# Kernel tuning notes

Measured on AMD Instinct MI355X. Metric: run time of the kernel, lower is better.

Reference implementation:

```python
import jax, jax.numpy as jnp
import numpy as np

B, S, E, H = 2, 2048, 768, 12
HD = E // H  # 64


def setup_inputs() -> dict:
    rng = jax.random.key(0)
    ks = jax.random.split(rng, 11)
    std = 0.02
    return {
        "query": jax.random.normal(ks[0], (B, S, E), dtype=jnp.float32),
        "key": jax.random.normal(ks[1], (B, S, E), dtype=jnp.float32),
        "value": jax.random.normal(ks[2], (B, S, E), dtype=jnp.float32),
        # weights stored as (in, out) so projection is x @ W + b
        "Wq": jax.random.normal(ks[3], (E, E), dtype=jnp.float32) * std,
        "bq": jax.random.normal(ks[4], (E,), dtype=jnp.float32) * std,
        "Wk": jax.random.normal(ks[5], (E, E), dtype=jnp.float32) * std,
        "bk": jax.random.normal(ks[6], (E,), dtype=jnp.float32) * std,
        "Wv": jax.random.normal(ks[7], (E, E), dtype=jnp.float32) * std,
        "bv": jax.random.normal(ks[8], (E,), dtype=jnp.float32) * std,
        "Wo": jax.random.normal(ks[9], (E, E), dtype=jnp.float32) * std,
        "bo": jax.random.normal(ks[10], (E,), dtype=jnp.float32) * std,
    }


def reference(query, key, value, Wq, bq, Wk, bk, Wv, bv, Wo, bo):
    bsz, tgt_len, embed_dim = query.shape
    src_len = key.shape[1]
    q = query @ Wq + bq  # [B, T, E]
    k = key @ Wk + bk    # [B, S, E]
    v = value @ Wv + bv  # [B, S, E]
    # Faithful replication of torch .view(bsz*H, len, head_dim) on a
    # (bsz, len, E)-contiguous tensor: plain row-major reshape (NOT a
    # transpose-based head split).
    q = q.reshape(bsz * H, tgt_len, HD)
    k = k.reshape(bsz * H, src_len, HD)
    v = v.reshape(bsz * H, src_len, HD)
    scale = 1.0 / (HD ** 0.5)
    scores = jnp.einsum('bqd,bkd->bqk', q, k) * scale  # [B*H, T, S]
    attn = jax.nn.softmax(scores, axis=-1)
    # is_causal=True: mask applied AFTER softmax (rows no longer normalized)
    attn = jnp.tril(attn)
    out = jnp.einsum('bqk,bkd->bqd', attn, v)  # [B*H, T, HD]
    out = out.reshape(bsz, tgt_len, embed_dim)
    return out @ Wo + bo
```

## Files before the change

kernel.cpp:

```cpp
#include <hip/hip_runtime.h>
#include <hip/hip_bf16.h>


typedef __bf16 bf16;
typedef __attribute__((ext_vector_type(4))) __bf16 bf16x4;
typedef __attribute__((ext_vector_type(8))) __bf16 bf16x8;
typedef __attribute__((ext_vector_type(4))) float f32x4;
typedef __attribute__((ext_vector_type(16))) float f32x16;
typedef __attribute__((ext_vector_type(4))) unsigned int uint4v;

#define MFMA16(a,b,c) __builtin_amdgcn_mfma_f32_16x16x32_bf16((a),(b),(c),0,0,0)
#define MFMA32(a,b,c) __builtin_amdgcn_mfma_f32_32x32x16_bf16((a),(b),(c),0,0,0)

typedef const __attribute__((address_space(1))) unsigned int GU32;
typedef __attribute__((address_space(3))) unsigned int LU32;

__device__ __forceinline__ void gll16(const void* gsrc, void* ldst) {
    __builtin_amdgcn_global_load_lds((GU32*)gsrc, (LU32*)ldst, 16, 0, 0);
}

__device__ __forceinline__ unsigned pk_bf16(float lo, float hi) {
    unsigned r;
    asm("v_cvt_pk_bf16_f32 %0, %1, %2" : "=v"(r) : "v"(lo), "v"(hi));
    return r;
}

__device__ __forceinline__ void plane32swap(unsigned &a, unsigned &b) {
    asm("v_permlane32_swap_b32 %0, %1" : "+v"(a), "+v"(b));
}

__device__ __forceinline__ bf16x8 frag_words(unsigned w0, unsigned w1, unsigned w2, unsigned w3) {
    union { unsigned u[4]; bf16x8 v; } f;
    f.u[0] = w0; f.u[1] = w1; f.u[2] = w2; f.u[3] = w3;
    return f.v;
}

__global__ __launch_bounds__(256) void cvt_qkv(
    const float* __restrict__ q, const float* __restrict__ k, const float* __restrict__ v,
    bf16* __restrict__ Qb, bf16* __restrict__ Kb, bf16* __restrict__ Vb)
{
    const float* src = blockIdx.y == 0 ? q : blockIdx.y == 1 ? k : v;
    bf16* dst = blockIdx.y == 0 ? Qb : blockIdx.y == 1 ? Kb : Vb;
    const size_t base = (size_t)blockIdx.x * 2048 + (size_t)threadIdx.x * 8;
    f32x4 lo = *(const f32x4*)&src[base];
    f32x4 hi = *(const f32x4*)&src[base + 4];
    bf16x8 o;
    for (int j = 0; j < 4; ++j) { o[j] = (bf16)lo[j]; o[4 + j] = (bf16)hi[j]; }
    *(bf16x8*)&dst[base] = o;
}

struct TArg { const float* in; bf16* out; };

__global__ __launch_bounds__(256) void transpose_w(TArg a0, TArg a1, TArg a2, TArg a3) {
    TArg ta = blockIdx.z == 0 ? a0 : blockIdx.z == 1 ? a1 : blockIdx.z == 2 ? a2 : a3;
    __shared__ bf16 tile[64][72];
    const int bx = blockIdx.x % 12, by = blockIdx.x / 12;
    const int k0 = by * 64, n0 = bx * 64;
    const int tid = threadIdx.x;
    for (int q = 0; q < 2; ++q) {
        int idx = q * 256 + tid;
        int i = idx >> 3, j0 = (idx & 7) * 8;
        const float* src = &ta.in[(size_t)(k0 + i) * 768 + n0 + j0];
        f32x4 lo = *(const f32x4*)&src[0];
        f32x4 hi = *(const f32x4*)&src[4];
        bf16x8 v;
        for (int j = 0; j < 4; ++j) { v[j] = (bf16)lo[j]; v[4 + j] = (bf16)hi[j]; }
        *(bf16x8*)&tile[i][j0] = v;
    }
    __syncthreads();
    for (int q = 0; q < 2; ++q) {
        int idx = q * 256 + tid;
        int n = idx >> 3, j0 = (idx & 7) * 8;
        bf16x8 v;
        for (int jj = 0; jj < 8; ++jj) v[jj] = tile[j0 + jj][n];
        *(bf16x8*)&ta.out[(size_t)(n0 + n) * 768 + k0 + j0] = v;
    }
}

__global__ __launch_bounds__(256) void vtrans(const bf16* __restrict__ Vp, bf16* __restrict__ Vt) {
    __shared__ bf16 tile[64][72];
    const int g = blockIdx.y;
    const int k0 = blockIdx.x * 64;
    const bf16* src = Vp + (size_t)g * 131072;
    bf16* dst = Vt + (size_t)g * 131072;
    const int tid = threadIdx.x;
    for (int q = 0; q < 2; ++q) {
        int idx = q * 256 + tid;
        int r = idx >> 3, c = (idx & 7) * 8;
        *(uint4v*)&tile[r][c] = *(const uint4v*)&src[(size_t)(k0 + r) * 64 + c];
    }
    __syncthreads();
    for (int q = 0; q < 2; ++q) {
        int idx = q * 256 + tid;
        int d = idx >> 3, c = (idx & 7) * 8;
        bf16x8 v;
        for (int j = 0; j < 8; ++j) v[j] = tile[c + j][d];
        *(bf16x8*)&dst[(size_t)d * 2048 + k0 + c] = v;
    }
}

struct GArg { const bf16* A; const bf16* Bt; const float* bias; void* C; float scale; };

template<int MODE>
__global__ __launch_bounds__(256) void gemm_bt_bias(GArg g0, GArg g1, GArg g2) {
    const int flat = blockIdx.x + 6 * blockIdx.y + 192 * blockIdx.z;
    const int xcd = flat & 7;
    const int idx = flat >> 3;
    const int mat = idx / 24;
    const int rem = idx % 24;
    const int rloc = rem / 6, colb = rem % 6;
    GArg ga = mat == 0 ? g0 : mat == 1 ? g1 : g2;
    const int K = 768, N = 768;
    __shared__ bf16 As[2][128][64];
    __shared__ bf16 Bs[2][128][64];
    const int tid = threadIdx.x;
    const int lane = tid & 63, wave = tid >> 6;
    const int l15 = lane & 15, lg = lane >> 4;
    const int r0 = (xcd * 4 + rloc) * 128, c0 = colb * 128;
    const int wr = (wave >> 1) * 64, wc = (wave & 1) * 64;
    f32x4 acc[4][4] = {};

    const int grow = wave * 8 + (lane >> 3);
    const int gcol = 8 * ((lane & 7) ^ (lane >> 3));

    auto stage = [&](int kt, int buf) {
        for (int i = 0; i < 4; ++i)
            gll16(&ga.A[(size_t)(r0 + i * 32 + grow) * K + kt + gcol], &As[buf][i * 32 + wave * 8][0]);
        for (int i = 0; i < 4; ++i)
            gll16(&ga.Bt[(size_t)(c0 + i * 32 + grow) * K + kt + gcol], &Bs[buf][i * 32 + wave * 8][0]);
    };

    stage(0, 0);
    __syncthreads();

    for (int c = 0; c < 12; ++c) {
        const int buf = c & 1;
        if (c < 11) stage((c + 1) * 64, buf ^ 1);
        for (int kk = 0; kk < 2; ++kk) {
            bf16x8 af[4], bfr[4];
            for (int i = 0; i < 4; ++i) {
                int row = wr + i * 16 + l15;
                af[i] = *(const bf16x8*)&As[buf][row][(kk * 32 + lg * 8) ^ ((row & 7) * 8)];
            }
            for (int j = 0; j < 4; ++j) {
                int row = wc + j * 16 + l15;
                bfr[j] = *(const bf16x8*)&Bs[buf][row][(kk * 32 + lg * 8) ^ ((row & 7) * 8)];
            }
            __builtin_amdgcn_s_setprio(1);
            for (int i = 0; i < 4; ++i)
                for (int j = 0; j < 4; ++j)
                    acc[i][j] = MFMA16(af[i], bfr[j], acc[i][j]);
            __builtin_amdgcn_s_setprio(0);
        }
        __syncthreads();
    }
    for (int j = 0; j < 4; ++j) {
        int col = c0 + wc + j * 16 + l15;
        float bv = ga.bias[col];
        for (int i = 0; i < 4; ++i) {
            int row = r0 + wr + i * 16 + lg * 4;
            for (int r = 0; r < 4; ++r) {
                float val = (acc[i][j][r] + bv) * ga.scale;
                if constexpr (MODE == 0)
                    ((bf16*)ga.C)[(size_t)(row + r) * N + col] = (bf16)val;
                else
                    ((float*)ga.C)[(size_t)(row + r) * N + col] = val;
            }
        }
    }
}

__global__ __launch_bounds__(256, 3) void attn_kernel(
    const bf16* __restrict__ Qp, const bf16* __restrict__ Kp,
    const bf16* __restrict__ Vtg, bf16* __restrict__ Ob)
{
    const int bid = blockIdx.x;
    const int xcd = bid & 7;
    const int idx = bid >> 3;
    const int t = idx & 31, s = idx >> 5;
    const int bx = (s == 0) ? (31 - t)
                 : (s == 1) ? ((15 - t) & 31)
                 : (((t << 1) & 31) | (t >> 4));
    const int g = xcd * 3 + s;
    const int t0 = bx * 64;
    const int tid = threadIdx.x, lane = tid & 63, w = tid >> 6;
    const int wq = w >> 1, p = w & 1;
    const int l31 = lane & 31, hi = lane >> 5;

    if (s == 1) __builtin_amdgcn_s_sleep(8);
    else if (s == 2) __builtin_amdgcn_s_sleep(16);

    __shared__ __align__(16) char smem[32768];
    bf16* KsE = (bf16*)smem;
    bf16* VsE = (bf16*)(smem + 16384);

    const bf16* Qg = Qp + (size_t)g * 131072;
    const bf16* Kg = Kp + (size_t)g * 131072;
    const bf16* Vg = Vtg + (size_t)g * 131072;
    bf16* Og = Ob + (size_t)g * 131072;

    const int qrow = t0 + wq * 32 + l31;
    bf16x8 qB[4];
    for (int m = 0; m < 4; ++m)
        qB[m] = *(const bf16x8*)&Qg[(size_t)qrow * 64 + m * 16 + hi * 8];

    const int srow = w * 16 + (lane >> 3);
    const int scol = 8 * ((lane & 7) ^ (lane >> 3));
    auto stageK = [&](int ch, int b2) {
        const bf16* src = &Kg[(size_t)(ch * 64 + srow) * 64 + scol];
        bf16* dst = KsE + b2 * 4096 + w * 16 * 64;
        gll16(src, dst);
        gll16(src + 8 * 64, dst + 8 * 64);
    };
    auto stageV = [&](int ch, int b2) {
        const bf16* src = &Vg[(size_t)srow * 2048 + ch * 64 + scol];
        bf16* dst = VsE + b2 * 4096 + w * 16 * 64;
        gll16(src, dst);
        gll16(src + 8 * 2048, dst + 8 * 64);
    };

    stageK(0, 0);
    stageV(0, 0);

    f32x16 oacc0 = {}, oacc1 = {};
    float dsum = 0.f;
    const int qmax = t0 + wq * 32 + 31;
    const int qmin = t0 + wq * 32;
    const int kofs = p * 32;
    const int swz = (l31 & 7) * 8;

    int koff[4], voff0[2], voff1[2];
    for (int m = 0; m < 4; ++m)
        koff[m] = (kofs + l31) * 64 + ((m * 16 + hi * 8) ^ swz);
    for (int kt = 0; kt < 2; ++kt) {
        const int col = (kofs + kt * 16 + hi * 8) ^ swz;
        voff0[kt] = l31 * 64 + col;
        voff1[kt] = (32 + l31) * 64 + col;
    }

    for (int c = 0; c < 32; ++c) {
        const int boff = (c & 1) * 4096;
        asm volatile("s_waitcnt vmcnt(0)" ::: "memory");
        __builtin_amdgcn_s_barrier();
        __builtin_amdgcn_sched_barrier(0);
        if (c < 31) {
            stageK(c + 1, (c & 1) ^ 1);
            if (c + 1 <= bx) stageV(c + 1, (c & 1) ^ 1);
        }
        __builtin_amdgcn_sched_barrier(0);

        const int kc = c * 64;
        const bool activ = (kc + kofs <= qmax);
        const bool fullc = (kc + kofs + 31 <= qmin);

        f32x16 s2 = {};
        __builtin_amdgcn_s_setprio(1);
        for (int m = 0; m < 4; ++m) {
            bf16x8 kf = *(const bf16x8*)&KsE[boff + koff[m]];
            s2 = MFMA32(kf, qB[m], s2);
        }
        __builtin_amdgcn_s_setprio(0);

        float e[16];
        for (int r = 0; r < 16; ++r) e[r] = __builtin_exp2f(s2[r]);
        {
            float p01 = e[0] + e[1],  p23 = e[2] + e[3];
            float p45 = e[4] + e[5],  p67 = e[6] + e[7];
            float p89 = e[8] + e[9],  pab = e[10] + e[11];
            float pcd = e[12] + e[13], pef = e[14] + e[15];
            float q0 = p01 + p23, q1 = p45 + p67, q2 = p89 + pab, q3 = pcd + pef;
            dsum += (q0 + q1) + (q2 + q3);
        }

        if (activ) {
            if (!fullc) {
                for (int r = 0; r < 16; ++r) {
                    int kg = kc + kofs + (r & 3) + 8 * (r >> 2) + 4 * hi;
                    if (kg > qrow) e[r] = 0.f;
                }
            }
            bf16x8 pf[2];
            {
                unsigned a0 = pk_bf16(e[0], e[1]), a1 = pk_bf16(e[2], e[3]);
                unsigned b0 = pk_bf16(e[4], e[5]), b1 = pk_bf16(e[6], e[7]);
                plane32swap(a0, b0); plane32swap(a1, b1);
                pf[0] = frag_words(a0, a1, b0, b1);
                a0 = pk_bf16(e[8], e[9]);   a1 = pk_bf16(e[10], e[11]);
                b0 = pk_bf16(e[12], e[13]); b1 = pk_bf16(e[14], e[15]);
                plane32swap(a0, b0); plane32swap(a1, b1);
                pf[1] = frag_words(a0, a1, b0, b1);
            }
            __builtin_amdgcn_s_setprio(1);
            for (int kt = 0; kt < 2; ++kt) {
                bf16x8 v0 = *(const bf16x8*)&VsE[boff + voff0[kt]];
                bf16x8 v1 = *(const bf16x8*)&VsE[boff + voff1[kt]];
                oacc0 = MFMA32(pf[kt], v0, oacc0);
                oacc1 = MFMA32(pf[kt], v1, oacc1);
            }
            __builtin_amdgcn_s_setprio(0);
        }
    }

    dsum += __shfl_xor(dsum, 32);

    __syncthreads();
    float* Ored = (float*)smem;
    float* dred = (float*)(smem + 16384);
    if (l31 == lane) dred[w * 32 + l31] = dsum;
    if (p == 1) {
        float* Op = Ored + wq * 2048;
        for (int r = 0; r < 16; ++r) {
            const int qoff = (r & 3) + 8 * (r >> 2) + 4 * hi;
            Op[qoff * 64 + l31]      = oacc0[r];
            Op[qoff * 64 + 32 + l31] = oacc1[r];
        }
    }
    __syncthreads();
    if (p == 0) {
        const float dtot = dsum + dred[(w + 1) * 32 + l31];
        const float rall = 1.0f / dtot;
        const float* Op = Ored + wq * 2048;
        for (int r = 0; r < 16; ++r) {
            const int qoff = (r & 3) + 8 * (r >> 2) + 4 * hi;
            const float inv = __shfl(rall, qoff);
            const size_t row = (size_t)(t0 + wq * 32 + qoff) * 64;
            Og[row + l31]      = (bf16)((oacc0[r] + Op[qoff * 64 + l31])      * inv);
            Og[row + 32 + l31] = (bf16)((oacc1[r] + Op[qoff * 64 + 32 + l31]) * inv);
        }
    }
}

extern "C" void kernel_launch(void* const* d_in, const int* in_sizes, int n_in,
                              void* d_out, int out_size, void* d_ws, size_t ws_size,
                              hipStream_t stream) {
    const float* query = (const float*)d_in[0];
    const float* key_  = (const float*)d_in[1];
    const float* value = (const float*)d_in[2];
    const float* Wq = (const float*)d_in[3];
    const float* bq = (const float*)d_in[4];
    const float* Wk = (const float*)d_in[5];
    const float* bk = (const float*)d_in[6];
    const float* Wv = (const float*)d_in[7];
    const float* bv = (const float*)d_in[8];
    const float* Wo = (const float*)d_in[9];
    const float* bo = (const float*)d_in[10];
    float* out = (float*)d_out;

    const size_t MN = (size_t)4096 * 768;
    const size_t WW = (size_t)768 * 768;
    bf16* Qp  = (bf16*)d_ws;
    bf16* Kp  = Qp + MN;
    bf16* Vp  = Kp + MN;
    bf16* Obf = Vp + MN;
    bf16* Vtg = Obf + MN;
    bf16* WtQ = Vtg + MN;
    bf16* WtK = WtQ + WW;
    bf16* WtV = WtK + WW;
    bf16* WtO = WtV + WW;
    bf16* Vb  = WtO + WW;
    bf16* Qb  = Obf;
    bf16* Kb  = Vtg;

    cvt_qkv<<<dim3(1536, 3), 256, 0, stream>>>(query, key_, value, Qb, Kb, Vb);

    transpose_w<<<dim3(144, 1, 4), 256, 0, stream>>>(
        TArg{Wq, WtQ}, TArg{Wk, WtK}, TArg{Wv, WtV}, TArg{Wo, WtO});

    gemm_bt_bias<0><<<dim3(6, 32, 3), 256, 0, stream>>>(
        GArg{Qb, WtQ, bq, Qp, 0.18033688f},
        GArg{Kb, WtK, bk, Kp, 1.0f},
        GArg{Vb, WtV, bv, Vp, 1.0f});

    vtrans<<<dim3(32, 24), 256, 0, stream>>>(Vp, Vtg);

    attn_kernel<<<dim3(768), 256, 0, stream>>>(Qp, Kp, Vtg, Obf);

    gemm_bt_bias<1><<<dim3(6, 32, 1), 256, 0, stream>>>(
        GArg{Obf, WtO, bo, out, 1.0f},
        GArg{Obf, WtO, bo, out, 1.0f},
        GArg{Obf, WtO, bo, out, 1.0f});
}
```

Baseline: 107.2 us.

## Merge input conversion and weight transpose kernels; fuse V transpose into projection epilogue

The separate fp32-to-bf16 conversion and weight-transpose kernels are merged into a single prelude launch that dispatches on block index. The V-projection GEMM epilogue now writes directly in the transposed per-head layout the attention kernel expects, removing the standalone vtrans kernel. This saves two launches and one full read and write of V. The transposed epilogue stores are scattered 2-byte writes with a stride of 2048 elements, so they are poorly coalesced.

```diff
diff --git a/kernel.cpp b/kernel.cpp
--- a/kernel.cpp
+++ b/kernel.cpp
@@ -35,71 +35,54 @@
     return f.v;
 }
 
-__global__ __launch_bounds__(256) void cvt_qkv(
+struct TArg { const float* in; bf16* out; };
+
+__global__ __launch_bounds__(256) void prelude(
     const float* __restrict__ q, const float* __restrict__ k, const float* __restrict__ v,
-    bf16* __restrict__ Qb, bf16* __restrict__ Kb, bf16* __restrict__ Vb)
+    bf16* __restrict__ Qb, bf16* __restrict__ Kb, bf16* __restrict__ Vb,
+    TArg a0, TArg a1, TArg a2, TArg a3)
 {
-    const float* src = blockIdx.y == 0 ? q : blockIdx.y == 1 ? k : v;
-    bf16* dst = blockIdx.y == 0 ? Qb : blockIdx.y == 1 ? Kb : Vb;
-    const size_t base = (size_t)blockIdx.x * 2048 + (size_t)threadIdx.x * 8;
-    f32x4 lo = *(const f32x4*)&src[base];
-    f32x4 hi = *(const f32x4*)&src[base + 4];
-    bf16x8 o;
-    for (int j = 0; j < 4; ++j) { o[j] = (bf16)lo[j]; o[4 + j] = (bf16)hi[j]; }
-    *(bf16x8*)&dst[base] = o;
-}
-
-struct TArg { const float* in; bf16* out; };
-
-__global__ __launch_bounds__(256) void transpose_w(TArg a0, TArg a1, TArg a2, TArg a3) {
-    TArg ta = blockIdx.z == 0 ? a0 : blockIdx.z == 1 ? a1 : blockIdx.z == 2 ? a2 : a3;
     __shared__ bf16 tile[64][72];
-    const int bx = blockIdx.x % 12, by = blockIdx.x / 12;
-    const int k0 = by * 64, n0 = bx * 64;
+    const int b = blockIdx.x;
     const int tid = threadIdx.x;
-    for (int q = 0; q < 2; ++q) {
-        int idx = q * 256 + tid;
-        int i = idx >> 3, j0 = (idx & 7) * 8;
-        const float* src = &ta.in[(size_t)(k0 + i) * 768 + n0 + j0];
-        f32x4 lo = *(const f32x4*)&src[0];
-        f32x4 hi = *(const f32x4*)&src[4];
-        bf16x8 v;
-        for (int j = 0; j < 4; ++j) { v[j] = (bf16)lo[j]; v[4 + j] = (bf16)hi[j]; }
-        *(bf16x8*)&tile[i][j0] = v;
-    }
-    __syncthreads();
-    for (int q = 0; q < 2; ++q) {
-        int idx = q * 256 + tid;
-        int n = idx >> 3, j0 = (idx & 7) * 8;
-        bf16x8 v;
-        for (int jj = 0; jj < 8; ++jj) v[jj] = tile[j0 + jj][n];
-        *(bf16x8*)&ta.out[(size_t)(n0 + n) * 768 + k0 + j0] = v;
-    }
-}
-
-__global__ __launch_bounds__(256) void vtrans(const bf16* __restrict__ Vp, bf16* __restrict__ Vt) {
-    __shared__ bf16 tile[64][72];
-    const int g = blockIdx.y;
-    const int k0 = blockIdx.x * 64;
-    const bf16* src = Vp + (size_t)g * 131072;
-    bf16* dst = Vt + (size_t)g * 131072;
-    const int tid = threadIdx.x;
-    for (int q = 0; q < 2; ++q) {
-        int idx = q * 256 + tid;
-        int r = idx >> 3, c = (idx & 7) * 8;
-        *(uint4v*)&tile[r][c] = *(const uint4v*)&src[(size_t)(k0 + r) * 64 + c];
-    }
-    __syncthreads();
-    for (int q = 0; q < 2; ++q) {
-        int idx = q * 256 + tid;
-        int d = idx >> 3, c = (idx & 7) * 8;
-        bf16x8 v;
-        for (int j = 0; j < 8; ++j) v[j] = tile[c + j][d];
-        *(bf16x8*)&dst[(size_t)d * 2048 + k0 + c] = v;
-    }
-}
-
-struct GArg { const bf16* A; const bf16* Bt; const float* bias; void* C; float scale; };
+    if (b < 4608) {
+        const int m = b / 1536, xx = b % 1536;
+        const float* src = m == 0 ? q : m == 1 ? k : v;
+        bf16* dst = m == 0 ? Qb : m == 1 ? Kb : Vb;
+        const size_t base = (size_t)xx * 2048 + (size_t)tid * 8;
+        f32x4 lo = *(const f32x4*)&src[base];
+        f32x4 hi = *(const f32x4*)&src[base + 4];
+        bf16x8 o;
+        for (int j = 0; j < 4; ++j) { o[j] = (bf16)lo[j]; o[4 + j] = (bf16)hi[j]; }
+        *(bf16x8*)&dst[base] = o;
+    } else {
+        const int bb = b - 4608;
+        const int wz = bb / 144, bxy = bb % 144;
+        TArg ta = wz == 0 ? a0 : wz == 1 ? a1 : wz == 2 ? a2 : a3;
+        const int bx = bxy % 12, by = bxy / 12;
+        const int k0 = by * 64, n0 = bx * 64;
+        for (int qq = 0; qq < 2; ++qq) {
+            int idx = qq * 256 + tid;
+            int i = idx >> 3, j0 = (idx & 7) * 8;
+            const float* src = &ta.in[(size_t)(k0 + i) * 768 + n0 + j0];
+            f32x4 lo = *(const f32x4*)&src[0];
+            f32x4 hi = *(const f32x4*)&src[4];
+            bf16x8 vv;
+            for (int j = 0; j < 4; ++j) { vv[j] = (bf16)lo[j]; vv[4 + j] = (bf16)hi[j]; }
+            *(bf16x8*)&tile[i][j0] = vv;
+        }
+        __syncthreads();
+        for (int qq = 0; qq < 2; ++qq) {
+            int idx = qq * 256 + tid;
+            int n = idx >> 3, j0 = (idx & 7) * 8;
+            bf16x8 vv;
+            for (int jj = 0; jj < 8; ++jj) vv[jj] = tile[j0 + jj][n];
+            *(bf16x8*)&ta.out[(size_t)(n0 + n) * 768 + k0 + j0] = vv;
+        }
+    }
+}
+
+struct GArg { const bf16* A; const bf16* Bt; const float* bias; void* C; float scale; int vt; };
 
 template<int MODE>
 __global__ __launch_bounds__(256) void gemm_bt_bias(GArg g0, GArg g1, GArg g2) {
@@ -154,6 +137,24 @@
         }
         __syncthreads();
     }
+
+    if (MODE == 0 && ga.vt) {
+        for (int j = 0; j < 4; ++j) {
+            int col = c0 + wc + j * 16 + l15;
+            float bv = ga.bias[col];
+            const int hh = col >> 6, d = col & 63;
+            for (int i = 0; i < 4; ++i) {
+                int row = r0 + wr + i * 16 + lg * 4;
+                for (int r = 0; r < 4; ++r) {
+                    int sidx = (row + r) * 12 + hh;
+                    int gq = sidx >> 11, kq = sidx & 2047;
+                    ((bf16*)ga.C)[(size_t)gq * 131072 + (size_t)d * 2048 + kq] =
+                        (bf16)(acc[i][j][r] + bv);
+                }
+            }
+        }
+        return;
+    }
     for (int j = 0; j < 4; ++j) {
         int col = c0 + wc + j * 16 + l15;
         float bv = ga.bias[col];
@@ -350,33 +351,30 @@
     const size_t WW = (size_t)768 * 768;
     bf16* Qp  = (bf16*)d_ws;
     bf16* Kp  = Qp + MN;
-    bf16* Vp  = Kp + MN;
-    bf16* Obf = Vp + MN;
-    bf16* Vtg = Obf + MN;
-    bf16* WtQ = Vtg + MN;
+    bf16* Vt  = Kp + MN;
+    bf16* Obf = Vt + MN;
+    bf16* Sp1 = Obf + MN;
+    bf16* WtQ = Sp1 + MN;
     bf16* WtK = WtQ + WW;
     bf16* WtV = WtK + WW;
     bf16* WtO = WtV + WW;
     bf16* Vb  = WtO + WW;
     bf16* Qb  = Obf;
-    bf16* Kb  = Vtg;
-
-    cvt_qkv<<<dim3(1536, 3), 256, 0, stream>>>(query, key_, value, Qb, Kb, Vb);
-
-    transpose_w<<<dim3(144, 1, 4), 256, 0, stream>>>(
+    bf16* Kb  = Sp1;
+
+    prelude<<<dim3(5184), 256, 0, stream>>>(
+        query, key_, value, Qb, Kb, Vb,
         TArg{Wq, WtQ}, TArg{Wk, WtK}, TArg{Wv, WtV}, TArg{Wo, WtO});
 
     gemm_bt_bias<0><<<dim3(6, 32, 3), 256, 0, stream>>>(
-        GArg{Qb, WtQ, bq, Qp, 0.18033688f},
-        GArg{Kb, WtK, bk, Kp, 1.0f},
-        GArg{Vb, WtV, bv, Vp, 1.0f});
-
-    vtrans<<<dim3(32, 24), 256, 0, stream>>>(Vp, Vtg);
-
-    attn_kernel<<<dim3(768), 256, 0, stream>>>(Qp, Kp, Vtg, Obf);
+        GArg{Qb, WtQ, bq, Qp, 0.18033688f, 0},
+        GArg{Kb, WtK, bk, Kp, 1.0f, 0},
+        GArg{Vb, WtV, bv, Vt, 1.0f, 1});
+
+    attn_kernel<<<dim3(768), 256, 0, stream>>>(Qp, Kp, Vt, Obf);
 
     gemm_bt_bias<1><<<dim3(6, 32, 1), 256, 0, stream>>>(
-        GArg{Obf, WtO, bo, out, 1.0f},
-        GArg{Obf, WtO, bo, out, 1.0f},
-        GArg{Obf, WtO, bo, out, 1.0f});
-}
+        GArg{Obf, WtO, bo, out, 1.0f, 0},
+        GArg{Obf, WtO, bo, out, 1.0f, 0},
+        GArg{Obf, WtO, bo, out, 1.0f, 0});
+}
```

Result: slower. 118.9 us (+10.9%).
